# Kernel optimization log

Hardware: AMD Instinct MI355X
Metric: run time of the kernel (lower is better)

## Reference

```python
import jax, jax.numpy as jnp
import numpy as np

N_NODES = 100000
N_EDGES = 1200000
HID = 64
EDGE_DIM = 16
N_LAYERS = 3


def setup_inputs() -> dict:
    key = jax.random.key(0)
    ks = jax.random.split(key, 16)
    s = 0.1  # weight scale
    return {
        'node_features': jax.random.normal(ks[0], (N_NODES, HID), jnp.float32),
        'edge_index': jax.random.randint(ks[1], (2, N_EDGES), 0, N_NODES, jnp.int32),
        'edge_features': jax.random.normal(ks[2], (N_EDGES, EDGE_DIM), jnp.float32),
        'enc_W': jax.random.normal(ks[3], (HID, HID), jnp.float32) * s,
        'enc_b': jnp.zeros((HID,), jnp.float32),
        'msg_W1': jax.random.normal(ks[4], (N_LAYERS, 2 * HID + EDGE_DIM, HID), jnp.float32) * s,
        'msg_b1': jnp.zeros((N_LAYERS, HID), jnp.float32),
        'msg_W2': jax.random.normal(ks[5], (N_LAYERS, HID, HID), jnp.float32) * s,
        'msg_b2': jnp.zeros((N_LAYERS, HID), jnp.float32),
        'gru_Wih': jax.random.normal(ks[6], (N_LAYERS, HID, 3 * HID), jnp.float32) * s,
        'gru_Whh': jax.random.normal(ks[7], (N_LAYERS, HID, 3 * HID), jnp.float32) * s,
        'gru_bih': jnp.zeros((N_LAYERS, 3 * HID), jnp.float32),
        'gru_bhh': jnp.zeros((N_LAYERS, 3 * HID), jnp.float32),
        'ro_W1': jax.random.normal(ks[8], (HID, HID), jnp.float32) * s,
        'ro_b1': jnp.zeros((HID,), jnp.float32),
        'ro_W2': jax.random.normal(ks[9], (HID, HID), jnp.float32) * s,
        'ro_b2': jnp.zeros((HID,), jnp.float32),
    }


def _gru_cell(x, h, Wih, Whh, bih, bhh):
    # torch GRUCell, gate order (r, z, n)
    gi = x @ Wih + bih  # [N, 3H]
    gh = h @ Whh + bhh
    gi_r, gi_z, gi_n = jnp.split(gi, 3, axis=-1)
    gh_r, gh_z, gh_n = jnp.split(gh, 3, axis=-1)
    r = jax.nn.sigmoid(gi_r + gh_r)
    z = jax.nn.sigmoid(gi_z + gh_z)
    n = jnp.tanh(gi_n + r * gh_n)
    return (1.0 - z) * n + z * h


def reference(node_features, edge_index, edge_features, enc_W, enc_b,
              msg_W1, msg_b1, msg_W2, msg_b2,
              gru_Wih, gru_Whh, gru_bih, gru_bhh,
              ro_W1, ro_b1, ro_W2, ro_b2):
    src, dst = edge_index[0], edge_index[1]
    n_nodes = node_features.shape[0]
    h = node_features @ enc_W + enc_b  # node encoder (no relu in graph path)
    for l in range(N_LAYERS):
        cat = jnp.concatenate([h[src], h[dst], edge_features], axis=-1)  # [E, 2H+Ed]
        m = jax.nn.relu(cat @ msg_W1[l] + msg_b1[l]) @ msg_W2[l] + msg_b2[l]  # [E, H]
        agg = jax.ops.segment_sum(m, dst, num_segments=n_nodes)  # scatter-add
        h = _gru_cell(agg, h, gru_Wih[l], gru_Whh[l], gru_bih[l], gru_bhh[l])
    return jax.nn.relu(h @ ro_W1 + ro_b1) @ ro_W2 + ro_b2
```

## Files before the change

kernel.cpp:

```cpp
#include <hip/hip_runtime.h>
#include <hip/hip_bf16.h>
#include <math.h>

#define HIDDIM 64
#define EDIM 16

typedef _Float16 h16;
typedef __attribute__((ext_vector_type(8))) _Float16 half8v;
typedef __attribute__((ext_vector_type(2))) _Float16 half2v;
typedef __attribute__((ext_vector_type(4))) float f32x4;
typedef unsigned int uint32;

#if defined(__has_builtin)
#if __has_builtin(__builtin_amdgcn_fdot2)
#define HAS_FDOT2 1
#endif
#endif

template<int K, int N, int EPI, int RELU, int AF32>
__global__ __launch_bounds__(256) void mfma_gemm_kernel(
    const float* __restrict__ A0f, const h16* __restrict__ A0h,
    const h16* __restrict__ A1h, const h16* __restrict__ Bp,
    const float* __restrict__ bias, float* __restrict__ outf,
    h16* __restrict__ outh, h16* __restrict__ outQ, h16* __restrict__ hbuf,
    const int* __restrict__ row_start, const float* __restrict__ b2ih, int M)
{
    constexpr int KP = K + 8;
    constexpr int NT = N / 16;
    constexpr int KC = K / 32;
    __shared__ __align__(16) h16 Asub[64 * KP];

    const int mbase = blockIdx.x * 64;
    const int tid = threadIdx.x;
    const int wid = tid >> 6, lane = tid & 63;

    constexpr int C8 = K / 8;
    constexpr int ITERS = 64 * C8 / 256;
#pragma unroll
    for (int it = 0; it < ITERS; ++it) {
        int idx = tid + it * 256;
        int row = idx / C8;
        int col = (idx - row * C8) * 8;
        int grow = mbase + row;
        half8v hv;
        if (grow < M) {
            if (AF32) {
                const float* sp = A0f + (size_t)grow * K + col;
                f32x4 a = *(const f32x4*)sp;
                f32x4 b = *(const f32x4*)(sp + 4);
                hv[0]=(h16)a.x; hv[1]=(h16)a.y; hv[2]=(h16)a.z; hv[3]=(h16)a.w;
                hv[4]=(h16)b.x; hv[5]=(h16)b.y; hv[6]=(h16)b.z; hv[7]=(h16)b.w;
            } else {
                const h16* sp;
                if (EPI == 3) {
                    sp = (col < 64) ? (A0h + (size_t)grow * 64 + col)
                                    : (A1h + (size_t)grow * 64 + (col - 64));
                } else {
                    sp = A0h + (size_t)grow * K + col;
                }
                hv = *(const half8v*)sp;
            }
        } else {
#pragma unroll
            for (int i = 0; i < 8; ++i) hv[i] = (h16)0.f;
        }
        *(half8v*)&Asub[row * KP + col] = hv;
    }
    __syncthreads();

    const int colb = lane & 15;
    f32x4 acc[NT];
#pragma unroll
    for (int t = 0; t < NT; ++t) {
        float bv = bias ? bias[t * 16 + colb] : 0.f;
        acc[t].x = bv; acc[t].y = bv; acc[t].z = bv; acc[t].w = bv;
    }
    const int aoff = (wid * 16 + colb) * KP + (lane >> 4) * 8;
    const half8v* Bv = (const half8v*)Bp;
#pragma unroll
    for (int c = 0; c < KC; ++c) {
        half8v af = *(const half8v*)&Asub[aoff + c * 32];
#pragma unroll
        for (int t = 0; t < NT; ++t) {
            half8v bf = Bv[(t * KC + c) * 64 + lane];
            acc[t] = __builtin_amdgcn_mfma_f32_16x16x32_f16(af, bf, acc[t], 0, 0, 0);
        }
    }

    if (EPI == 0) {
#pragma unroll
        for (int r = 0; r < 4; ++r) {
            int row = mbase + wid * 16 + (lane >> 4) * 4 + r;
            if (row < M) {
#pragma unroll
                for (int t = 0; t < NT; ++t) {
                    float vv = acc[t][r];
                    if (RELU) vv = vv > 0.f ? vv : 0.f;
                    outf[(size_t)row * N + t * 16 + colb] = vv;
                }
            }
        }
    } else if (EPI == 1) {
#pragma unroll
        for (int r = 0; r < 4; ++r) {
            int row = mbase + wid * 16 + (lane >> 4) * 4 + r;
            if (row < M) {
#pragma unroll
                for (int t = 0; t < NT; ++t) {
                    float vv = acc[t][r];
                    if (RELU) vv = vv > 0.f ? vv : 0.f;
                    outh[(size_t)row * N + t * 16 + colb] = (h16)vv;
                }
            }
        }
    } else if (EPI == 2) {
#pragma unroll
        for (int r = 0; r < 4; ++r) {
            int row = mbase + wid * 16 + (lane >> 4) * 4 + r;
            if (row < M) {
#pragma unroll
                for (int t = 0; t < NT; ++t) {
                    h16 us = (h16)acc[t][r];
                    int col = t * 16 + colb;
                    if (t < 4) outh[(size_t)row * 64 + col] = us;
                    else       outQ[(size_t)row * 64 + (col - 64)] = us;
                }
            }
        }
    } else {
        float b2r[4], b2z[4], b2n[4];
#pragma unroll
        for (int j4 = 0; j4 < 4; ++j4) {
            int j = j4 * 16 + colb;
            b2r[j4] = b2ih[j];
            b2z[j4] = b2ih[64 + j];
            b2n[j4] = b2ih[128 + j];
        }
#pragma unroll
        for (int r = 0; r < 4; ++r) {
            int row = mbase + wid * 16 + (lane >> 4) * 4 + r;
            if (row < M) {
                float deg = (float)(row_start[row + 1] - row_start[row]);
#pragma unroll
                for (int j4 = 0; j4 < 4; ++j4) {
                    float rv = acc[j4][r] + deg * b2r[j4];
                    rv = 1.f / (1.f + __expf(-rv));
                    float zv = acc[4 + j4][r] + deg * b2z[j4];
                    zv = 1.f / (1.f + __expf(-zv));
                    float gin = acc[8 + j4][r] + deg * b2n[j4];
                    float ghn = acc[12 + j4][r];
                    float nv = tanhf(gin + rv * ghn);
                    size_t off = (size_t)row * 64 + j4 * 16 + colb;
                    float hold = (float)hbuf[off];
                    hbuf[off] = (h16)((1.f - zv) * nv + zv * hold);
                }
            }
        }
    }
}

__global__ __launch_bounds__(256) void pack_plain_kernel(
    const float* __restrict__ B, h16* __restrict__ Bp, int Kd, int Nd)
{
    int idx = blockIdx.x * 256 + threadIdx.x;
    int KC = Kd >> 5;
    int total = (Nd >> 4) * KC * 64;
    if (idx >= total) return;
    int lane = idx & 63, fc = idx >> 6;
    int t = fc / KC, c = fc - t * KC;
    int col = t * 16 + (lane & 15);
    int k0 = c * 32 + (lane >> 4) * 8;
    half8v us;
#pragma unroll
    for (int i = 0; i < 8; ++i) us[i] = (h16)B[(size_t)(k0 + i) * Nd + col];
    *(half8v*)(Bp + (size_t)idx * 8) = us;
}

__global__ __launch_bounds__(256) void pack_pq_kernel(
    const float* __restrict__ W1, h16* __restrict__ Bp)
{
    int idx = blockIdx.x * 256 + threadIdx.x;
    if (idx >= 1024) return;
    int lane = idx & 63, fc = idx >> 6;
    int t = fc >> 1, c = fc & 1;
    int n = t * 16 + (lane & 15);
    int k0 = c * 32 + (lane >> 4) * 8;
    half8v us;
#pragma unroll
    for (int i = 0; i < 8; ++i) {
        int k = k0 + i;
        float v = (n < 64) ? W1[(size_t)k * 64 + n]
                           : W1[(size_t)(64 + k) * 64 + (n - 64)];
        us[i] = (h16)v;
    }
    *(half8v*)(Bp + (size_t)idx * 8) = us;
}

__global__ __launch_bounds__(256) void pack_gru_kernel(
    const float* __restrict__ Wci, const float* __restrict__ Whh,
    h16* __restrict__ Bp)
{
    int idx = blockIdx.x * 256 + threadIdx.x;
    if (idx >= 4096) return;
    int lane = idx & 63, fc = idx >> 6;
    int t = fc >> 2, c = fc & 3;
    int n = t * 16 + (lane & 15);
    int k0 = c * 32 + (lane >> 4) * 8;
    half8v us;
#pragma unroll
    for (int i = 0; i < 8; ++i) {
        int k = k0 + i;
        float v;
        if (n < 128)      v = (k < 64) ? Wci[(size_t)k * 192 + n]
                                       : Whh[(size_t)(k - 64) * 192 + n];
        else if (n < 192) v = (k < 64) ? Wci[(size_t)k * 192 + n] : 0.f;
        else              v = (k >= 64) ? Whh[(size_t)(k - 64) * 192 + (n - 64)] : 0.f;
        us[i] = (h16)v;
    }
    *(half8v*)(Bp + (size_t)idx * 8) = us;
}

__global__ __launch_bounds__(256) void pack_w1c_kernel(
    const float* __restrict__ mW1, h16* __restrict__ w1ch)
{
    int idx = blockIdx.x * 256 + threadIdx.x;
    if (idx >= 3 * 1024) return;
    int l = idx >> 10, r = idx & 1023;
    w1ch[idx] = (h16)mW1[(size_t)l * 144 * 64 + 128 * 64 + r];
}

__global__ void bias_pq_kernel(const float* __restrict__ b1, float* __restrict__ out)
{
    int i = threadIdx.x;
    out[i] = (i < 64) ? 0.f : b1[i - 64];
}

__global__ void bias_gru_kernel(const float* __restrict__ bih,
                                const float* __restrict__ bhh,
                                float* __restrict__ out)
{
    int i = threadIdx.x;
    float v;
    if (i < 128)      v = bih[i] + bhh[i];
    else if (i < 192) v = bih[i];
    else              v = bhh[i - 64];
    out[i] = v;
}

__global__ __launch_bounds__(256) void count_kernel(
    const int* __restrict__ dst, int* __restrict__ cnt, int nE)
{
    int e = blockIdx.x * 256 + threadIdx.x;
    if (e >= nE) return;
    atomicAdd(&cnt[dst[e]], 1);
}

__global__ __launch_bounds__(256) void partial_kernel(
    const int* __restrict__ cnt, int* __restrict__ partial, int nNodes)
{
    __shared__ int lds[256];
    int i = blockIdx.x * 256 + threadIdx.x;
    int v = (i < nNodes) ? cnt[i] : 0;
    lds[threadIdx.x] = v;
    __syncthreads();
#pragma unroll
    for (int off = 128; off > 0; off >>= 1) {
        if (threadIdx.x < off) lds[threadIdx.x] += lds[threadIdx.x + off];
        __syncthreads();
    }
    if (threadIdx.x == 0) partial[blockIdx.x] = lds[0];
}

__global__ __launch_bounds__(1024) void scan_partials_kernel(
    int* __restrict__ partial, int* __restrict__ row_start, int nb,
    int nNodes, int nE)
{
    __shared__ int lds[1024];
    int tid = threadIdx.x;
    int v = (tid < nb) ? partial[tid] : 0;
    lds[tid] = v;
    __syncthreads();
    for (int off = 1; off < 1024; off <<= 1) {
        int t = (tid >= off) ? lds[tid - off] : 0;
        __syncthreads();
        lds[tid] += t;
        __syncthreads();
    }
    if (tid < nb) partial[tid] = lds[tid] - v;
    if (tid == 0) row_start[nNodes] = nE;
}

__global__ __launch_bounds__(256) void scan_blocks_kernel(
    const int* __restrict__ cnt, const int* __restrict__ partial,
    int* __restrict__ row_start, int* __restrict__ cursor, int nNodes)
{
    __shared__ int lds[256];
    int i = blockIdx.x * 256 + threadIdx.x;
    int v = (i < nNodes) ? cnt[i] : 0;
    lds[threadIdx.x] = v;
    __syncthreads();
    for (int off = 1; off < 256; off <<= 1) {
        int t = (threadIdx.x >= off) ? lds[threadIdx.x - off] : 0;
        __syncthreads();
        lds[threadIdx.x] += t;
        __syncthreads();
    }
    if (i < nNodes) {
        int excl = partial[blockIdx.x] + lds[threadIdx.x] - v;
        row_start[i] = excl;
        cursor[i] = excl;
    }
}

__global__ __launch_bounds__(256) void fill_kernel(
    const int* __restrict__ src, const int* __restrict__ dst,
    const float* __restrict__ ef, int* __restrict__ cursor,
    int* __restrict__ ss, h16* __restrict__ sefh, int nE)
{
    int e = blockIdx.x * 256 + threadIdx.x;
    if (e >= nE) return;
    int d = dst[e];
    int p = atomicAdd(&cursor[d], 1);
    ss[p] = src[e];
    const float4* er = reinterpret_cast<const float4*>(ef + (size_t)e * 16);
    float4 a0 = er[0], a1 = er[1], a2 = er[2], a3 = er[3];
    half8v u0, u1;
    u0[0]=(h16)a0.x; u0[1]=(h16)a0.y; u0[2]=(h16)a0.z; u0[3]=(h16)a0.w;
    u0[4]=(h16)a1.x; u0[5]=(h16)a1.y; u0[6]=(h16)a1.z; u0[7]=(h16)a1.w;
    u1[0]=(h16)a2.x; u1[1]=(h16)a2.y; u1[2]=(h16)a2.z; u1[3]=(h16)a2.w;
    u1[4]=(h16)a3.x; u1[5]=(h16)a3.y; u1[6]=(h16)a3.z; u1[7]=(h16)a3.w;
    half8v* sr = reinterpret_cast<half8v*>(sefh + (size_t)p * 16);
    sr[0] = u0; sr[1] = u1;
}

__global__ void combine_kernel(
    const float* __restrict__ mW2, const float* __restrict__ mb2,
    const float* __restrict__ gWih, float* __restrict__ Wci,
    float* __restrict__ b2ih)
{
    int l = blockIdx.x;
    int g = threadIdx.x;
    const float* W2  = mW2  + (size_t)l * 64 * 64;
    const float* Wih = gWih + (size_t)l * 64 * 192;
    const float* b2  = mb2  + (size_t)l * 64;
    float acc[64];
#pragma unroll
    for (int k = 0; k < 64; ++k) acc[k] = 0.f;
    float bacc = 0.f;
#pragma unroll 1
    for (int j = 0; j < 64; ++j) {
        float w = Wih[j * 192 + g];
        bacc += b2[j] * w;
#pragma unroll
        for (int k = 0; k < 64; ++k) acc[k] += W2[k * 64 + j] * w;
    }
    float* o = Wci + (size_t)l * 64 * 192;
#pragma unroll
    for (int k = 0; k < 64; ++k) o[k * 192 + g] = acc[k];
    b2ih[l * 192 + g] = bacc;
}

__device__ __forceinline__ float edot16(half8v a, half8v b, const half2v w[8],
                                        float seed)
{
    float r = seed;
#if defined(HAS_FDOT2)
    const half2v* ap = (const half2v*)&a;
    const half2v* bp = (const half2v*)&b;
#pragma unroll
    for (int j = 0; j < 4; ++j) r = __builtin_amdgcn_fdot2(ap[j], w[j], r, false);
#pragma unroll
    for (int j = 0; j < 4; ++j) r = __builtin_amdgcn_fdot2(bp[j], w[4 + j], r, false);
#else
#pragma unroll
    for (int k = 0; k < 8; ++k) r += (float)a[k] * (float)w[k >> 1][k & 1];
#pragma unroll
    for (int k = 0; k < 8; ++k) r += (float)b[k] * (float)w[4 + (k >> 1)][k & 1];
#endif
    return r;
}

__global__ __launch_bounds__(256) void edge_agg_kernel(
    const h16* __restrict__ Pb, const h16* __restrict__ Qb,
    h16* __restrict__ T, const h16* __restrict__ sefh,
    const h16* __restrict__ w1ch, const int* __restrict__ sorted_src,
    const int* __restrict__ row_start, int nNodes)
{
    int wg = blockIdx.x * 4 + (threadIdx.x >> 6);
    wg = __builtin_amdgcn_readfirstlane(wg);
    int lane = threadIdx.x & 63;
    int nw = gridDim.x * 4;

    half2v w2[8];
#pragma unroll
    for (int j = 0; j < 8; ++j) {
        half2v p;
        p[0] = w1ch[(2 * j) * 64 + lane];
        p[1] = w1ch[(2 * j + 1) * 64 + lane];
        w2[j] = p;
    }

    for (int n = wg; n < nNodes; n += nw) {
        int rs = row_start[n];
        int re = row_start[n + 1];
        float q = (float)Qb[(size_t)n * 64 + lane];
        float tacc = 0.f;
        int i = rs;
        for (; i + 8 <= re; i += 8) {
            float p[8];
#pragma unroll
            for (int j = 0; j < 8; ++j) {
                int s = sorted_src[i + j];
                p[j] = (float)Pb[(size_t)s * 64 + lane];
            }
            const half8v* e8 = reinterpret_cast<const half8v*>(sefh + (size_t)i * 16);
#pragma unroll
            for (int j = 0; j < 8; ++j) {
                float t = edot16(e8[2 * j], e8[2 * j + 1], w2, p[j] + q);
                t = t > 0.f ? t : 0.f;
                tacc += t;
            }
        }
        for (; i + 4 <= re; i += 4) {
            float p[4];
#pragma unroll
            for (int j = 0; j < 4; ++j) {
                int s = sorted_src[i + j];
                p[j] = (float)Pb[(size_t)s * 64 + lane];
            }
            const half8v* e8 = reinterpret_cast<const half8v*>(sefh + (size_t)i * 16);
#pragma unroll
            for (int j = 0; j < 4; ++j) {
                float t = edot16(e8[2 * j], e8[2 * j + 1], w2, p[j] + q);
                t = t > 0.f ? t : 0.f;
                tacc += t;
            }
        }
        for (; i < re; ++i) {
            int s = sorted_src[i];
            float p = (float)Pb[(size_t)s * 64 + lane];
            const half8v* e8 = reinterpret_cast<const half8v*>(sefh + (size_t)i * 16);
            float t = edot16(e8[0], e8[1], w2, p + q);
            t = t > 0.f ? t : 0.f;
            tacc += t;
        }
        T[(size_t)n * 64 + lane] = (h16)tacc;
    }
}

extern "C" void kernel_launch(void* const* d_in, const int* in_sizes, int n_in,
                              void* d_out, int out_size, void* d_ws, size_t ws_size,
                              hipStream_t stream)
{
    const float* nf    = (const float*)d_in[0];
    const int*   ei    = (const int*)  d_in[1];
    const float* ef    = (const float*)d_in[2];
    const float* enc_W = (const float*)d_in[3];
    const float* enc_b = (const float*)d_in[4];
    const float* mW1   = (const float*)d_in[5];
    const float* mb1   = (const float*)d_in[6];
    const float* mW2   = (const float*)d_in[7];
    const float* mb2   = (const float*)d_in[8];
    const float* gWih  = (const float*)d_in[9];
    const float* gWhh  = (const float*)d_in[10];
    const float* gbih  = (const float*)d_in[11];
    const float* gbhh  = (const float*)d_in[12];
    const float* rW1   = (const float*)d_in[13];
    const float* rb1   = (const float*)d_in[14];
    const float* rW2   = (const float*)d_in[15];
    const float* rb2   = (const float*)d_in[16];

    const int N = in_sizes[0] / HIDDIM;
    const int E = in_sizes[2] / EDIM;

    char* wsB = (char*)d_ws;
    auto alloc = [&](size_t bytes) {
        char* p = wsB;
        wsB += (bytes + 255) & ~(size_t)255;
        return p;
    };
    h16*  h           = (h16*)alloc((size_t)N * 64 * 2);
    h16*  T           = (h16*)alloc((size_t)N * 64 * 2);
    h16*  Rt          = (h16*)alloc((size_t)N * 64 * 2);
    h16*  Pb          = (h16*)alloc((size_t)N * 64 * 2);
    h16*  Qb          = (h16*)alloc((size_t)N * 64 * 2);
    int*   row_start  = (int*)alloc((size_t)(N + 1) * 4);
    int*   cursor     = (int*)alloc((size_t)N * 4);
    int*   cnt        = (int*)alloc((size_t)N * 4);
    int*   partial    = (int*)alloc(1024 * 4);
    int*   s_src      = (int*)alloc((size_t)E * 4);
    h16*  sefh        = (h16*)alloc((size_t)E * 16 * 2);
    float* Wci        = (float*)alloc(3 * 64 * 192 * 4);
    float* b2ih       = (float*)alloc(3 * 192 * 4);
    h16*  encP        = (h16*)alloc(512 * 8 * 2);
    h16*  pqP         = (h16*)alloc(3 * 1024 * 8 * 2);
    h16*  gruP        = (h16*)alloc(3 * 4096 * 8 * 2);
    h16*  ro1P        = (h16*)alloc(512 * 8 * 2);
    h16*  ro2P        = (h16*)alloc(512 * 8 * 2);
    h16*  w1ch        = (h16*)alloc(3 * 1024 * 2);
    float* bias128    = (float*)alloc(3 * 128 * 4);
    float* bias256    = (float*)alloc(3 * 256 * 4);

    const int gemmGrid = (N + 63) / 64;
    const int edgeGrid = (E + 255) / 256;
    const int nScanBlk = (N + 255) / 256;

    hipMemsetAsync(cnt, 0, (size_t)N * 4, stream);
    count_kernel<<<edgeGrid, 256, 0, stream>>>(ei + E, cnt, E);
    partial_kernel<<<nScanBlk, 256, 0, stream>>>(cnt, partial, N);
    scan_partials_kernel<<<1, 1024, 0, stream>>>(partial, row_start, nScanBlk, N, E);
    scan_blocks_kernel<<<nScanBlk, 256, 0, stream>>>(cnt, partial, row_start, cursor, N);
    fill_kernel<<<edgeGrid, 256, 0, stream>>>(ei, ei + E, ef, cursor, s_src, sefh, E);

    combine_kernel<<<3, 192, 0, stream>>>(mW2, mb2, gWih, Wci, b2ih);
    pack_plain_kernel<<<2, 256, 0, stream>>>(enc_W, encP, 64, 64);
    pack_plain_kernel<<<2, 256, 0, stream>>>(rW1, ro1P, 64, 64);
    pack_plain_kernel<<<2, 256, 0, stream>>>(rW2, ro2P, 64, 64);
    pack_w1c_kernel<<<12, 256, 0, stream>>>(mW1, w1ch);
    for (int l = 0; l < 3; ++l) {
        pack_pq_kernel<<<4, 256, 0, stream>>>(mW1 + (size_t)l * 144 * 64,
                                              pqP + (size_t)l * 1024 * 8);
        pack_gru_kernel<<<16, 256, 0, stream>>>(Wci + (size_t)l * 64 * 192,
                                                gWhh + (size_t)l * 64 * 192,
                                                gruP + (size_t)l * 4096 * 8);
        bias_pq_kernel<<<1, 128, 0, stream>>>(mb1 + (size_t)l * 64,
                                              bias128 + (size_t)l * 128);
        bias_gru_kernel<<<1, 256, 0, stream>>>(gbih + (size_t)l * 192,
                                               gbhh + (size_t)l * 192,
                                               bias256 + (size_t)l * 256);
    }

    mfma_gemm_kernel<64, 64, 1, 0, 1><<<gemmGrid, 256, 0, stream>>>(
        nf, nullptr, nullptr, encP, enc_b, nullptr, h, nullptr, nullptr,
        nullptr, nullptr, N);

    for (int l = 0; l < 3; ++l) {
        mfma_gemm_kernel<64, 128, 2, 0, 0><<<gemmGrid, 256, 0, stream>>>(
            nullptr, h, nullptr, pqP + (size_t)l * 1024 * 8,
            bias128 + (size_t)l * 128, nullptr, Pb, Qb, nullptr,
            nullptr, nullptr, N);
        edge_agg_kernel<<<2048, 256, 0, stream>>>(
            Pb, Qb, T, sefh, w1ch + (size_t)l * 1024, s_src, row_start, N);
        mfma_gemm_kernel<128, 256, 3, 0, 0><<<gemmGrid, 256, 0, stream>>>(
            nullptr, T, h, gruP + (size_t)l * 4096 * 8,
            bias256 + (size_t)l * 256, nullptr, nullptr, nullptr, h,
            row_start, b2ih + (size_t)l * 192, N);
    }

    mfma_gemm_kernel<64, 64, 1, 1, 0><<<gemmGrid, 256, 0, stream>>>(
        nullptr, h, nullptr, ro1P, rb1, nullptr, Rt, nullptr, nullptr,
        nullptr, nullptr, N);
    mfma_gemm_kernel<64, 64, 0, 0, 0><<<gemmGrid, 256, 0, stream>>>(
        nullptr, Rt, nullptr, ro2P, rb2, (float*)d_out, nullptr, nullptr,
        nullptr, nullptr, nullptr, N);
}
```

Before: 824.6 us.

## Fuse node GEMM chains: encoder+PQ, GRU+next-layer PQ, GRU+readout MLP

Replaces the generic templated GEMM kernel with three fused kernels that keep intermediate node tiles in shared memory. The encoder output feeds the first layer's P/Q projection directly, each GRU update feeds the next layer's P/Q projection, and the last GRU runs the two-layer readout MLP in the same kernel. Weight-packing and bias kernels are batched across layers to cut launch count. This removes global round-trips of h and Rt and several launches, at the cost of more shared memory and registers per block, which may lower occupancy.

```diff
diff --git a/kernel.cpp b/kernel.cpp
--- a/kernel.cpp
+++ b/kernel.cpp
@@ -17,171 +17,312 @@
 #endif
 #endif
 
-template<int K, int N, int EPI, int RELU, int AF32>
-__global__ __launch_bounds__(256) void mfma_gemm_kernel(
-    const float* __restrict__ A0f, const h16* __restrict__ A0h,
-    const h16* __restrict__ A1h, const h16* __restrict__ Bp,
-    const float* __restrict__ bias, float* __restrict__ outf,
-    h16* __restrict__ outh, h16* __restrict__ outQ, h16* __restrict__ hbuf,
-    const int* __restrict__ row_start, const float* __restrict__ b2ih, int M)
-{
-    constexpr int KP = K + 8;
-    constexpr int NT = N / 16;
-    constexpr int KC = K / 32;
-    __shared__ __align__(16) h16 Asub[64 * KP];
-
+template<int KP, int KC, int NT>
+__device__ __forceinline__ void run_mfma(const h16* Asub, const h16* Bp,
+                                         f32x4* acc, int wid, int lane)
+{
+    const int colb = lane & 15;
+    const int aoff = (wid * 16 + colb) * KP + (lane >> 4) * 8;
+    const half8v* Bv = (const half8v*)Bp;
+#pragma unroll
+    for (int c = 0; c < KC; ++c) {
+        half8v af = *(const half8v*)&Asub[aoff + c * 32];
+#pragma unroll
+        for (int t = 0; t < NT; ++t) {
+            half8v bf = Bv[(t * KC + c) * 64 + lane];
+            acc[t] = __builtin_amdgcn_mfma_f32_16x16x32_f16(af, bf, acc[t], 0, 0, 0);
+        }
+    }
+}
+
+template<int NT>
+__device__ __forceinline__ void init_acc(f32x4* acc, const float* bias, int lane)
+{
+    const int colb = lane & 15;
+#pragma unroll
+    for (int t = 0; t < NT; ++t) {
+        float bv = bias ? bias[t * 16 + colb] : 0.f;
+        acc[t].x = bv; acc[t].y = bv; acc[t].z = bv; acc[t].w = bv;
+    }
+}
+
+__global__ __launch_bounds__(256) void enc_pq_kernel(
+    const float* __restrict__ nf, const h16* __restrict__ encP,
+    const float* __restrict__ enc_b, const h16* __restrict__ pqP0,
+    const float* __restrict__ bias128_0, h16* __restrict__ hout,
+    h16* __restrict__ Pb, h16* __restrict__ Qb, int M)
+{
+    __shared__ __align__(16) h16 Asub[64 * 72];
+    __shared__ __align__(16) h16 Htile[64 * 72];
     const int mbase = blockIdx.x * 64;
     const int tid = threadIdx.x;
     const int wid = tid >> 6, lane = tid & 63;
-
-    constexpr int C8 = K / 8;
-    constexpr int ITERS = 64 * C8 / 256;
-#pragma unroll
-    for (int it = 0; it < ITERS; ++it) {
+    const int colb = lane & 15;
+
+#pragma unroll
+    for (int it = 0; it < 2; ++it) {
         int idx = tid + it * 256;
-        int row = idx / C8;
-        int col = (idx - row * C8) * 8;
+        int row = idx >> 3;
+        int col = (idx & 7) * 8;
         int grow = mbase + row;
         half8v hv;
         if (grow < M) {
-            if (AF32) {
-                const float* sp = A0f + (size_t)grow * K + col;
-                f32x4 a = *(const f32x4*)sp;
-                f32x4 b = *(const f32x4*)(sp + 4);
-                hv[0]=(h16)a.x; hv[1]=(h16)a.y; hv[2]=(h16)a.z; hv[3]=(h16)a.w;
-                hv[4]=(h16)b.x; hv[5]=(h16)b.y; hv[6]=(h16)b.z; hv[7]=(h16)b.w;
-            } else {
-                const h16* sp;
-                if (EPI == 3) {
-                    sp = (col < 64) ? (A0h + (size_t)grow * 64 + col)
-                                    : (A1h + (size_t)grow * 64 + (col - 64));
-                } else {
-                    sp = A0h + (size_t)grow * K + col;
-                }
-                hv = *(const half8v*)sp;
+            const float* sp = nf + (size_t)grow * 64 + col;
+            f32x4 a = *(const f32x4*)sp;
+            f32x4 b = *(const f32x4*)(sp + 4);
+            hv[0]=(h16)a.x; hv[1]=(h16)a.y; hv[2]=(h16)a.z; hv[3]=(h16)a.w;
+            hv[4]=(h16)b.x; hv[5]=(h16)b.y; hv[6]=(h16)b.z; hv[7]=(h16)b.w;
+        } else {
+#pragma unroll
+            for (int i = 0; i < 8; ++i) hv[i] = (h16)0.f;
+        }
+        *(half8v*)&Asub[row * 72 + col] = hv;
+    }
+    __syncthreads();
+
+    f32x4 acc[4];
+    init_acc<4>(acc, enc_b, lane);
+    run_mfma<72, 2, 4>(Asub, encP, acc, wid, lane);
+
+#pragma unroll
+    for (int r = 0; r < 4; ++r) {
+        int lrow = wid * 16 + (lane >> 4) * 4 + r;
+        int grow = mbase + lrow;
+#pragma unroll
+        for (int t = 0; t < 4; ++t) {
+            h16 v = (h16)acc[t][r];
+            Htile[lrow * 72 + t * 16 + colb] = v;
+            if (grow < M) hout[(size_t)grow * 64 + t * 16 + colb] = v;
+        }
+    }
+    __syncthreads();
+
+    f32x4 acc2[8];
+    init_acc<8>(acc2, bias128_0, lane);
+    run_mfma<72, 2, 8>(Htile, pqP0, acc2, wid, lane);
+
+#pragma unroll
+    for (int r = 0; r < 4; ++r) {
+        int grow = mbase + wid * 16 + (lane >> 4) * 4 + r;
+        if (grow < M) {
+#pragma unroll
+            for (int t = 0; t < 8; ++t) {
+                h16 us = (h16)acc2[t][r];
+                int col = t * 16 + colb;
+                if (t < 4) Pb[(size_t)grow * 64 + col] = us;
+                else       Qb[(size_t)grow * 64 + (col - 64)] = us;
             }
+        }
+    }
+}
+
+__global__ __launch_bounds__(256) void gru_pq_kernel(
+    const h16* __restrict__ T, h16* __restrict__ h,
+    const h16* __restrict__ gruP, const float* __restrict__ bias256,
+    const int* __restrict__ row_start, const float* __restrict__ b2ih,
+    const h16* __restrict__ pqPn, const float* __restrict__ bias128n,
+    h16* __restrict__ Pb, h16* __restrict__ Qb, int M)
+{
+    __shared__ __align__(16) h16 Asub[64 * 136];
+    __shared__ __align__(16) h16 Htile[64 * 72];
+    const int mbase = blockIdx.x * 64;
+    const int tid = threadIdx.x;
+    const int wid = tid >> 6, lane = tid & 63;
+    const int colb = lane & 15;
+
+#pragma unroll
+    for (int it = 0; it < 4; ++it) {
+        int idx = tid + it * 256;
+        int row = idx >> 4;
+        int col = (idx & 15) * 8;
+        int grow = mbase + row;
+        half8v hv;
+        if (grow < M) {
+            const h16* sp = (col < 64) ? (T + (size_t)grow * 64 + col)
+                                       : (h + (size_t)grow * 64 + (col - 64));
+            hv = *(const half8v*)sp;
         } else {
 #pragma unroll
             for (int i = 0; i < 8; ++i) hv[i] = (h16)0.f;
         }
-        *(half8v*)&Asub[row * KP + col] = hv;
-    }
-    __syncthreads();
-
+        *(half8v*)&Asub[row * 136 + col] = hv;
+    }
+    __syncthreads();
+
+    f32x4 acc[16];
+    init_acc<16>(acc, bias256, lane);
+    run_mfma<136, 4, 16>(Asub, gruP, acc, wid, lane);
+
+    float b2r[4], b2z[4], b2n[4];
+#pragma unroll
+    for (int j4 = 0; j4 < 4; ++j4) {
+        int j = j4 * 16 + colb;
+        b2r[j4] = b2ih[j]; b2z[j4] = b2ih[64 + j]; b2n[j4] = b2ih[128 + j];
+    }
+#pragma unroll
+    for (int r = 0; r < 4; ++r) {
+        int lrow = wid * 16 + (lane >> 4) * 4 + r;
+        int grow = mbase + lrow;
+        float deg = (grow < M) ? (float)(row_start[grow + 1] - row_start[grow]) : 0.f;
+#pragma unroll
+        for (int j4 = 0; j4 < 4; ++j4) {
+            float rv = acc[j4][r] + deg * b2r[j4];
+            rv = 1.f / (1.f + __expf(-rv));
+            float zv = acc[4 + j4][r] + deg * b2z[j4];
+            zv = 1.f / (1.f + __expf(-zv));
+            float gin = acc[8 + j4][r] + deg * b2n[j4];
+            float ghn = acc[12 + j4][r];
+            float nv = tanhf(gin + rv * ghn);
+            float hold = (float)Asub[lrow * 136 + 64 + j4 * 16 + colb];
+            h16 hv = (h16)((1.f - zv) * nv + zv * hold);
+            Htile[lrow * 72 + j4 * 16 + colb] = hv;
+            if (grow < M) h[(size_t)grow * 64 + j4 * 16 + colb] = hv;
+        }
+    }
+    __syncthreads();
+
+    f32x4 acc2[8];
+    init_acc<8>(acc2, bias128n, lane);
+    run_mfma<72, 2, 8>(Htile, pqPn, acc2, wid, lane);
+
+#pragma unroll
+    for (int r = 0; r < 4; ++r) {
+        int grow = mbase + wid * 16 + (lane >> 4) * 4 + r;
+        if (grow < M) {
+#pragma unroll
+            for (int t = 0; t < 8; ++t) {
+                h16 us = (h16)acc2[t][r];
+                int col = t * 16 + colb;
+                if (t < 4) Pb[(size_t)grow * 64 + col] = us;
+                else       Qb[(size_t)grow * 64 + (col - 64)] = us;
+            }
+        }
+    }
+}
+
+__global__ __launch_bounds__(256) void gru_ro_kernel(
+    const h16* __restrict__ T, const h16* __restrict__ h,
+    const h16* __restrict__ gruP, const float* __restrict__ bias256,
+    const int* __restrict__ row_start, const float* __restrict__ b2ih,
+    const h16* __restrict__ ro1P, const float* __restrict__ rb1,
+    const h16* __restrict__ ro2P, const float* __restrict__ rb2,
+    float* __restrict__ out, int M)
+{
+    __shared__ __align__(16) h16 Asub[64 * 136];
+    __shared__ __align__(16) h16 Htile[64 * 72];
+    const int mbase = blockIdx.x * 64;
+    const int tid = threadIdx.x;
+    const int wid = tid >> 6, lane = tid & 63;
     const int colb = lane & 15;
-    f32x4 acc[NT];
-#pragma unroll
-    for (int t = 0; t < NT; ++t) {
-        float bv = bias ? bias[t * 16 + colb] : 0.f;
-        acc[t].x = bv; acc[t].y = bv; acc[t].z = bv; acc[t].w = bv;
-    }
-    const int aoff = (wid * 16 + colb) * KP + (lane >> 4) * 8;
-    const half8v* Bv = (const half8v*)Bp;
-#pragma unroll
-    for (int c = 0; c < KC; ++c) {
-        half8v af = *(const half8v*)&Asub[aoff + c * 32];
-#pragma unroll
-        for (int t = 0; t < NT; ++t) {
-            half8v bf = Bv[(t * KC + c) * 64 + lane];
-            acc[t] = __builtin_amdgcn_mfma_f32_16x16x32_f16(af, bf, acc[t], 0, 0, 0);
-        }
-    }
-
-    if (EPI == 0) {
-#pragma unroll
-        for (int r = 0; r < 4; ++r) {
-            int row = mbase + wid * 16 + (lane >> 4) * 4 + r;
-            if (row < M) {
-#pragma unroll
-                for (int t = 0; t < NT; ++t) {
-                    float vv = acc[t][r];
-                    if (RELU) vv = vv > 0.f ? vv : 0.f;
-                    outf[(size_t)row * N + t * 16 + colb] = vv;
-                }
-            }
-        }
-    } else if (EPI == 1) {
-#pragma unroll
-        for (int r = 0; r < 4; ++r) {
-            int row = mbase + wid * 16 + (lane >> 4) * 4 + r;
-            if (row < M) {
-#pragma unroll
-                for (int t = 0; t < NT; ++t) {
-                    float vv = acc[t][r];
-                    if (RELU) vv = vv > 0.f ? vv : 0.f;
-                    outh[(size_t)row * N + t * 16 + colb] = (h16)vv;
-                }
-            }
-        }
-    } else if (EPI == 2) {
-#pragma unroll
-        for (int r = 0; r < 4; ++r) {
-            int row = mbase + wid * 16 + (lane >> 4) * 4 + r;
-            if (row < M) {
-#pragma unroll
-                for (int t = 0; t < NT; ++t) {
-                    h16 us = (h16)acc[t][r];
-                    int col = t * 16 + colb;
-                    if (t < 4) outh[(size_t)row * 64 + col] = us;
-                    else       outQ[(size_t)row * 64 + (col - 64)] = us;
-                }
-            }
-        }
-    } else {
-        float b2r[4], b2z[4], b2n[4];
+
+#pragma unroll
+    for (int it = 0; it < 4; ++it) {
+        int idx = tid + it * 256;
+        int row = idx >> 4;
+        int col = (idx & 15) * 8;
+        int grow = mbase + row;
+        half8v hv;
+        if (grow < M) {
+            const h16* sp = (col < 64) ? (T + (size_t)grow * 64 + col)
+                                       : (h + (size_t)grow * 64 + (col - 64));
+            hv = *(const half8v*)sp;
+        } else {
+#pragma unroll
+            for (int i = 0; i < 8; ++i) hv[i] = (h16)0.f;
+        }
+        *(half8v*)&Asub[row * 136 + col] = hv;
+    }
+    __syncthreads();
+
+    f32x4 acc[16];
+    init_acc<16>(acc, bias256, lane);
+    run_mfma<136, 4, 16>(Asub, gruP, acc, wid, lane);
+
+    float b2r[4], b2z[4], b2n[4];
+#pragma unroll
+    for (int j4 = 0; j4 < 4; ++j4) {
+        int j = j4 * 16 + colb;
+        b2r[j4] = b2ih[j]; b2z[j4] = b2ih[64 + j]; b2n[j4] = b2ih[128 + j];
+    }
+#pragma unroll
+    for (int r = 0; r < 4; ++r) {
+        int lrow = wid * 16 + (lane >> 4) * 4 + r;
+        int grow = mbase + lrow;
+        float deg = (grow < M) ? (float)(row_start[grow + 1] - row_start[grow]) : 0.f;
 #pragma unroll
         for (int j4 = 0; j4 < 4; ++j4) {
-            int j = j4 * 16 + colb;
-            b2r[j4] = b2ih[j];
-            b2z[j4] = b2ih[64 + j];
-            b2n[j4] = b2ih[128 + j];
-        }
-#pragma unroll
-        for (int r = 0; r < 4; ++r) {
-            int row = mbase + wid * 16 + (lane >> 4) * 4 + r;
-            if (row < M) {
-                float deg = (float)(row_start[row + 1] - row_start[row]);
-#pragma unroll
-                for (int j4 = 0; j4 < 4; ++j4) {
-                    float rv = acc[j4][r] + deg * b2r[j4];
-                    rv = 1.f / (1.f + __expf(-rv));
-                    float zv = acc[4 + j4][r] + deg * b2z[j4];
-                    zv = 1.f / (1.f + __expf(-zv));
-                    float gin = acc[8 + j4][r] + deg * b2n[j4];
-                    float ghn = acc[12 + j4][r];
-                    float nv = tanhf(gin + rv * ghn);
-                    size_t off = (size_t)row * 64 + j4 * 16 + colb;
-                    float hold = (float)hbuf[off];
-                    hbuf[off] = (h16)((1.f - zv) * nv + zv * hold);
-                }
-            }
-        }
-    }
-}
-
-__global__ __launch_bounds__(256) void pack_plain_kernel(
-    const float* __restrict__ B, h16* __restrict__ Bp, int Kd, int Nd)
+            float rv = acc[j4][r] + deg * b2r[j4];
+            rv = 1.f / (1.f + __expf(-rv));
+            float zv = acc[4 + j4][r] + deg * b2z[j4];
+            zv = 1.f / (1.f + __expf(-zv));
+            float gin = acc[8 + j4][r] + deg * b2n[j4];
+            float ghn = acc[12 + j4][r];
+            float nv = tanhf(gin + rv * ghn);
+            float hold = (float)Asub[lrow * 136 + 64 + j4 * 16 + colb];
+            Htile[lrow * 72 + j4 * 16 + colb] = (h16)((1.f - zv) * nv + zv * hold);
+        }
+    }
+    __syncthreads();
+
+    f32x4 acc2[4];
+    init_acc<4>(acc2, rb1, lane);
+    run_mfma<72, 2, 4>(Htile, ro1P, acc2, wid, lane);
+
+#pragma unroll
+    for (int r = 0; r < 4; ++r) {
+        int lrow = wid * 16 + (lane >> 4) * 4 + r;
+#pragma unroll
+        for (int t = 0; t < 4; ++t) {
+            float v = acc2[t][r];
+            v = v > 0.f ? v : 0.f;
+            Asub[lrow * 72 + t * 16 + colb] = (h16)v;
+        }
+    }
+    __syncthreads();
+
+    f32x4 acc3[4];
+    init_acc<4>(acc3, rb2, lane);
+    run_mfma<72, 2, 4>(Asub, ro2P, acc3, wid, lane);
+
+#pragma unroll
+    for (int r = 0; r < 4; ++r) {
+        int grow = mbase + wid * 16 + (lane >> 4) * 4 + r;
+        if (grow < M) {
+#pragma unroll
+            for (int t = 0; t < 4; ++t)
+                out[(size_t)grow * 64 + t * 16 + colb] = acc3[t][r];
+        }
+    }
+}
+
+__global__ __launch_bounds__(256) void pack_plain3_kernel(
+    const float* __restrict__ encW, const float* __restrict__ rW1,
+    const float* __restrict__ rW2, h16* __restrict__ encP,
+    h16* __restrict__ ro1P, h16* __restrict__ ro2P)
 {
     int idx = blockIdx.x * 256 + threadIdx.x;
-    int KC = Kd >> 5;
-    int total = (Nd >> 4) * KC * 64;
-    if (idx >= total) return;
-    int lane = idx & 63, fc = idx >> 6;
-    int t = fc / KC, c = fc - t * KC;
+    if (idx >= 1536) return;
+    int w = idx >> 9, u = idx & 511;
+    const float* B = (w == 0) ? encW : (w == 1) ? rW1 : rW2;
+    h16* Bp = (w == 0) ? encP : (w == 1) ? ro1P : ro2P;
+    int lane = u & 63, fc = u >> 6;
+    int t = fc >> 1, c = fc & 1;
     int col = t * 16 + (lane & 15);
     int k0 = c * 32 + (lane >> 4) * 8;
     half8v us;
 #pragma unroll
-    for (int i = 0; i < 8; ++i) us[i] = (h16)B[(size_t)(k0 + i) * Nd + col];
-    *(half8v*)(Bp + (size_t)idx * 8) = us;
-}
-
-__global__ __launch_bounds__(256) void pack_pq_kernel(
-    const float* __restrict__ W1, h16* __restrict__ Bp)
+    for (int i = 0; i < 8; ++i) us[i] = (h16)B[(size_t)(k0 + i) * 64 + col];
+    *(half8v*)(Bp + (size_t)u * 8) = us;
+}
+
+__global__ __launch_bounds__(256) void pack_pq_all_kernel(
+    const float* __restrict__ mW1, h16* __restrict__ pqP)
 {
     int idx = blockIdx.x * 256 + threadIdx.x;
-    if (idx >= 1024) return;
-    int lane = idx & 63, fc = idx >> 6;
+    if (idx >= 3 * 1024) return;
+    int l = idx >> 10, u = idx & 1023;
+    const float* W1 = mW1 + (size_t)l * 144 * 64;
+    int lane = u & 63, fc = u >> 6;
     int t = fc >> 1, c = fc & 1;
     int n = t * 16 + (lane & 15);
     int k0 = c * 32 + (lane >> 4) * 8;
@@ -193,16 +334,19 @@
                            : W1[(size_t)(64 + k) * 64 + (n - 64)];
         us[i] = (h16)v;
     }
-    *(half8v*)(Bp + (size_t)idx * 8) = us;
-}
-
-__global__ __launch_bounds__(256) void pack_gru_kernel(
-    const float* __restrict__ Wci, const float* __restrict__ Whh,
-    h16* __restrict__ Bp)
+    *(half8v*)(pqP + (size_t)idx * 8) = us;
+}
+
+__global__ __launch_bounds__(256) void pack_gru_all_kernel(
+    const float* __restrict__ Wci, const float* __restrict__ gWhh,
+    h16* __restrict__ gruP)
 {
     int idx = blockIdx.x * 256 + threadIdx.x;
-    if (idx >= 4096) return;
-    int lane = idx & 63, fc = idx >> 6;
+    if (idx >= 3 * 4096) return;
+    int l = idx >> 12, u = idx & 4095;
+    const float* Wc = Wci + (size_t)l * 64 * 192;
+    const float* Wh = gWhh + (size_t)l * 64 * 192;
+    int lane = u & 63, fc = u >> 6;
     int t = fc >> 2, c = fc & 3;
     int n = t * 16 + (lane & 15);
     int k0 = c * 32 + (lane >> 4) * 8;
@@ -211,13 +355,13 @@
     for (int i = 0; i < 8; ++i) {
         int k = k0 + i;
         float v;
-        if (n < 128)      v = (k < 64) ? Wci[(size_t)k * 192 + n]
-                                       : Whh[(size_t)(k - 64) * 192 + n];
-        else if (n < 192) v = (k < 64) ? Wci[(size_t)k * 192 + n] : 0.f;
-        else              v = (k >= 64) ? Whh[(size_t)(k - 64) * 192 + (n - 64)] : 0.f;
+        if (n < 128)      v = (k < 64) ? Wc[(size_t)k * 192 + n]
+                                       : Wh[(size_t)(k - 64) * 192 + n];
+        else if (n < 192) v = (k < 64) ? Wc[(size_t)k * 192 + n] : 0.f;
+        else              v = (k >= 64) ? Wh[(size_t)(k - 64) * 192 + (n - 64)] : 0.f;
         us[i] = (h16)v;
     }
-    *(half8v*)(Bp + (size_t)idx * 8) = us;
+    *(half8v*)(gruP + (size_t)idx * 8) = us;
 }
 
 __global__ __launch_bounds__(256) void pack_w1c_kernel(
@@ -229,22 +373,21 @@
     w1ch[idx] = (h16)mW1[(size_t)l * 144 * 64 + 128 * 64 + r];
 }
 
-__global__ void bias_pq_kernel(const float* __restrict__ b1, float* __restrict__ out)
-{
-    int i = threadIdx.x;
-    out[i] = (i < 64) ? 0.f : b1[i - 64];
-}
-
-__global__ void bias_gru_kernel(const float* __restrict__ bih,
-                                const float* __restrict__ bhh,
-                                float* __restrict__ out)
-{
-    int i = threadIdx.x;
+__global__ void bias_all_kernel(
+    const float* __restrict__ mb1, const float* __restrict__ gbih,
+    const float* __restrict__ gbhh, float* __restrict__ bias128,
+    float* __restrict__ bias256)
+{
+    int l = blockIdx.x, i = threadIdx.x;
+    if (i < 128)
+        bias128[l * 128 + i] = (i < 64) ? 0.f : mb1[l * 64 + i - 64];
+    const float* bih = gbih + l * 192;
+    const float* bhh = gbhh + l * 192;
     float v;
     if (i < 128)      v = bih[i] + bhh[i];
     else if (i < 192) v = bih[i];
     else              v = bhh[i - 64];
-    out[i] = v;
+    bias256[l * 256 + i] = v;
 }
 
 __global__ __launch_bounds__(256) void count_kernel(
@@ -481,7 +624,6 @@
     };
     h16*  h           = (h16*)alloc((size_t)N * 64 * 2);
     h16*  T           = (h16*)alloc((size_t)N * 64 * 2);
-    h16*  Rt          = (h16*)alloc((size_t)N * 64 * 2);
     h16*  Pb          = (h16*)alloc((size_t)N * 64 * 2);
     h16*  Qb          = (h16*)alloc((size_t)N * 64 * 2);
     int*   row_start  = (int*)alloc((size_t)(N + 1) * 4);
@@ -513,44 +655,29 @@
     fill_kernel<<<edgeGrid, 256, 0, stream>>>(ei, ei + E, ef, cursor, s_src, sefh, E);
 
     combine_kernel<<<3, 192, 0, stream>>>(mW2, mb2, gWih, Wci, b2ih);
-    pack_plain_kernel<<<2, 256, 0, stream>>>(enc_W, encP, 64, 64);
-    pack_plain_kernel<<<2, 256, 0, stream>>>(rW1, ro1P, 64, 64);
-    pack_plain_kernel<<<2, 256, 0, stream>>>(rW2, ro2P, 64, 64);
+    pack_plain3_kernel<<<6, 256, 0, stream>>>(enc_W, rW1, rW2, encP, ro1P, ro2P);
+    pack_pq_all_kernel<<<12, 256, 0, stream>>>(mW1, pqP);
+    pack_gru_all_kernel<<<48, 256, 0, stream>>>(Wci, gWhh, gruP);
     pack_w1c_kernel<<<12, 256, 0, stream>>>(mW1, w1ch);
-    for (int l = 0; l < 3; ++l) {
-        pack_pq_kernel<<<4, 256, 0, stream>>>(mW1 + (size_t)l * 144 * 64,
-                                              pqP + (size_t)l * 1024 * 8);
-        pack_gru_kernel<<<16, 256, 0, stream>>>(Wci + (size_t)l * 64 * 192,
-                                                gWhh + (size_t)l * 64 * 192,
-                                                gruP + (size_t)l * 4096 * 8);
-        bias_pq_kernel<<<1, 128, 0, stream>>>(mb1 + (size_t)l * 64,
-                                              bias128 + (size_t)l * 128);
-        bias_gru_kernel<<<1, 256, 0, stream>>>(gbih + (size_t)l * 192,
-                                               gbhh + (size_t)l * 192,
-                                               bias256 + (size_t)l * 256);
-    }
-
-    mfma_gemm_kernel<64, 64, 1, 0, 1><<<gemmGrid, 256, 0, stream>>>(
-        nf, nullptr, nullptr, encP, enc_b, nullptr, h, nullptr, nullptr,
-        nullptr, nullptr, N);
-
-    for (int l = 0; l < 3; ++l) {
-        mfma_gemm_kernel<64, 128, 2, 0, 0><<<gemmGrid, 256, 0, stream>>>(
-            nullptr, h, nullptr, pqP + (size_t)l * 1024 * 8,
-            bias128 + (size_t)l * 128, nullptr, Pb, Qb, nullptr,
-            nullptr, nullptr, N);
+    bias_all_kernel<<<3, 256, 0, stream>>>(mb1, gbih, gbhh, bias128, bias256);
+
+    enc_pq_kernel<<<gemmGrid, 256, 0, stream>>>(
+        nf, encP, enc_b, pqP, bias128, h, Pb, Qb, N);
+
+    for (int l = 0; l < 2; ++l) {
         edge_agg_kernel<<<2048, 256, 0, stream>>>(
             Pb, Qb, T, sefh, w1ch + (size_t)l * 1024, s_src, row_start, N);
-        mfma_gemm_kernel<128, 256, 3, 0, 0><<<gemmGrid, 256, 0, stream>>>(
-            nullptr, T, h, gruP + (size_t)l * 4096 * 8,
-            bias256 + (size_t)l * 256, nullptr, nullptr, nullptr, h,
-            row_start, b2ih + (size_t)l * 192, N);
-    }
-
-    mfma_gemm_kernel<64, 64, 1, 1, 0><<<gemmGrid, 256, 0, stream>>>(
-        nullptr, h, nullptr, ro1P, rb1, nullptr, Rt, nullptr, nullptr,
-        nullptr, nullptr, N);
-    mfma_gemm_kernel<64, 64, 0, 0, 0><<<gemmGrid, 256, 0, stream>>>(
-        nullptr, Rt, nullptr, ro2P, rb2, (float*)d_out, nullptr, nullptr,
-        nullptr, nullptr, nullptr, N);
-}
+        gru_pq_kernel<<<gemmGrid, 256, 0, stream>>>(
+            T, h, gruP + (size_t)l * 4096 * 8, bias256 + (size_t)l * 256,
+            row_start, b2ih + (size_t)l * 192,
+            pqP + (size_t)(l + 1) * 1024 * 8, bias128 + (size_t)(l + 1) * 128,
+            Pb, Qb, N);
+    }
+
+    edge_agg_kernel<<<2048, 256, 0, stream>>>(
+        Pb, Qb, T, sefh, w1ch + (size_t)2 * 1024, s_src, row_start, N);
+    gru_ro_kernel<<<gemmGrid, 256, 0, stream>>>(
+        T, h, gruP + (size_t)2 * 4096 * 8, bias256 + (size_t)2 * 256,
+        row_start, b2ih + (size_t)2 * 192,
+        ro1P, rb1, ro2P, rb2, (float*)d_out, N);
+}
```

New measurement: 786.2 us. 1.05x faster.
